# Optimization experiments

Hardware: AMD Instinct MI355X
Metric: run time of the kernel (lower is better)

Reference implementation:

```python
import jax, jax.numpy as jnp
import numpy as np

B, S, DM, DC, L, NS = 4, 2048, 2048, 512, 4, 5  # batch, seq, d_model, d_cortical, n_layers, n_settle


def _ln(x, g, b):
    # torch nn.LayerNorm, eps=1e-5
    m = x.mean(-1, keepdims=True)
    v = ((x - m) ** 2).mean(-1, keepdims=True)
    return (x - m) * jax.lax.rsqrt(v + 1e-5) * g + b


def setup_inputs() -> dict:
    key = jax.random.key(0)
    ks = jax.random.split(key, 20)
    f = lambda k, sh: jax.random.normal(k, sh, jnp.float32) * 0.02
    return dict(
        qwen_final_hidden=jax.random.normal(ks[0], (B, S, DM), jnp.float32),
        obs=jax.random.normal(ks[1], (4, B, S, DM), jnp.float32),
        proj_W=f(ks[2], (4, DC, DM)), proj_b=f(ks[3], (4, DC)),
        fuse_W=f(ks[4], (DC, 4 * DC)), fuse_b=f(ks[5], (DC,)),
        up_W=f(ks[6], (L, DC, DC)), up_b=f(ks[7], (L, DC)),
        lateral_W=f(ks[8], (L, DC, DC)), lateral_b=f(ks[9], (L, DC)),
        precision_logit=f(ks[10], (L, DC)),
        ln_g=jnp.ones((L, DC), jnp.float32), ln_b=jnp.zeros((L, DC), jnp.float32),
        down_W=f(ks[11], (L - 1, DC, DC)), down_b=f(ks[12], (L - 1, DC)),
        out1_W=f(ks[13], (DC, DC)), out1_b=f(ks[14], (DC,)),
        out2_W=f(ks[15], (DM, DC)), out2_b=f(ks[16], (DM,)),
    )


def reference(qwen_final_hidden, obs, proj_W, proj_b, fuse_W, fuse_b,
              up_W, up_b, lateral_W, lateral_b, precision_logit,
              ln_g, ln_b, down_W, down_b, out1_W, out1_b, out2_W, out2_b):
    b, s, dm = qwen_final_hidden.shape
    # per-observed-layer input projections, concatenated along features
    proj = jnp.einsum('obsd,ocd->bsoc', obs, proj_W) + proj_b  # (B,S,4,DC)
    cat = proj.reshape(b, s, -1)
    fused = cat @ fuse_W.T + fuse_b                             # (B,S,DC)
    x0 = fused.reshape(b * s, DC)                               # per-token cortical input

    prec = jax.nn.sigmoid(precision_logit)                      # (L,DC)

    # initial bottom-up pass: activations = compress(x)
    acts = []
    x = x0
    for i in range(L):
        x = _ln(x @ up_W[i].T + up_b[i], ln_g[i], ln_b[i])
        acts.append(x)

    # settling iterations
    for _ in range(NS):
        # top-down predictions computed from pre-sweep activations
        preds = [None] * L
        for i in range(L - 1, 0, -1):
            if i < L - 1:  # top layer has no top-down weights
                preds[i - 1] = acts[i] @ down_W[i].T + down_b[i]
        x = x0
        for i in range(L):
            compressed = _ln(x @ up_W[i].T + up_b[i], ln_g[i], ln_b[i])
            target = preds[i] if preds[i] is not None else acts[i]
            werr = (compressed - target) * prec[i]
            lateral = acts[i] @ lateral_W[i].T + lateral_b[i]
            acts[i] = _ln(acts[i] + 0.5 * werr + 0.1 * lateral, ln_g[i], ln_b[i])
            x = acts[i]

    top = acts[-1]
    h = jax.nn.gelu(top @ out1_W.T + out1_b, approximate=False)
    correction = (h @ out2_W.T + out2_b).reshape(b, s, dm)
    return qwen_final_hidden + correction
```

## Files before the change

### kernel.cpp

```cpp
#include <hip/hip_runtime.h>
#include <hip/hip_bf16.h>
#include <math.h>

#define NTOK 8192
#define DMD  2048
#define DCC  512
#define TOKH 4194304

typedef __attribute__((ext_vector_type(8))) short short8;
typedef __attribute__((ext_vector_type(4))) float f32x4;

__device__ inline float bf2f(unsigned short u) {
    union { unsigned int i; float f; } x; x.i = ((unsigned int)u) << 16; return x.f;
}
__device__ inline unsigned short f2bf(float f) {
    union { float f; unsigned int i; } x; x.f = f;
    unsigned int u = x.i;
    return (unsigned short)((u + 0x7fffu + ((u >> 16) & 1u)) >> 16);
}

typedef const __attribute__((address_space(1))) unsigned int* gas1_t;
typedef __attribute__((address_space(3))) unsigned int* las3_t;
__device__ inline void async16(const void* g, void* l) {
    __builtin_amdgcn_global_load_lds(
        (gas1_t)g,
        (las3_t)(unsigned int)(unsigned long long)l, 16, 0, 0);
}

__global__ __launch_bounds__(256)
void cvt_kernel(const float* __restrict__ s, unsigned short* __restrict__ d, int n4)
{
    int i = blockIdx.x * 256 + threadIdx.x;
    if (i >= n4) return;
    float4 v = ((const float4*)s)[i];
    ushort4 o;
    o.x = f2bf(v.x); o.y = f2bf(v.y); o.z = f2bf(v.z); o.w = f2bf(v.w);
    ((ushort4*)d)[i] = o;
}

struct CvtArgs { const float* src[7]; };

__global__ __launch_bounds__(256)
void wcvt_kernel(CvtArgs ca, unsigned short* __restrict__ dst)
{
    const int total = 2359296;
    for (int i = blockIdx.x * 256 + threadIdx.x; i < total; i += gridDim.x * 256) {
        const float* sp; int base;
        if      (i < 1048576) { sp = ca.src[0]; base = 0;       }
        else if (i < 1310720) { sp = ca.src[1]; base = 1048576; }
        else if (i < 1572864) { sp = ca.src[2]; base = 1310720; }
        else if (i < 1835008) { sp = ca.src[3]; base = 1572864; }
        else if (i < 2031616) { sp = ca.src[4]; base = 1835008; }
        else if (i < 2097152) { sp = ca.src[5]; base = 2031616; }
        else                  { sp = ca.src[6]; base = 2097152; }
        float4 v = ((const float4*)sp)[i - base];
        ushort4 o;
        o.x = f2bf(v.x); o.y = f2bf(v.y); o.z = f2bf(v.z); o.w = f2bf(v.w);
        ((ushort4*)dst)[i] = o;
    }
}

struct GArgs {
    const unsigned short* A[6];
    const unsigned short* W[6];
    const float*          bias[6];
    const float*          add[6];
    void*                 C[6];
};

template<bool OUTF32, bool GELU>
__global__ __launch_bounds__(256)
void gemm16(GArgs ga, int lda, int ldw, int ldadd, int ldc, int K)
{
    __shared__ unsigned short As[128 * 32];
    __shared__ unsigned short Bs[128 * 32];

    const int z    = blockIdx.z;
    const int tid  = threadIdx.x;
    const int wave = tid >> 6;
    const int lane = tid & 63;

    const int nwg   = gridDim.x * gridDim.y;
    const int bid   = blockIdx.y * gridDim.x + blockIdx.x;
    const int swz   = (bid & 7) * (nwg >> 3) + (bid >> 3);
    const int bn    = (swz % gridDim.x) * 128;
    const int bm    = (swz / gridDim.x) * 128;

    const int wr   = wave >> 1;
    const int wc   = wave & 1;

    const unsigned short* Ap = ga.A[z];
    const unsigned short* Wp = ga.W[z];

    const int lrow = lane >> 2;
    const int lcol = (lane & 3) * 8;

    f32x4 acc[4][4] = {};

    for (int k0 = 0; k0 < K; k0 += 32) {
        #pragma unroll
        for (int r = 0; r < 2; ++r) {
            int c = wave + r * 4;
            async16(Ap + (size_t)(bm + c * 16 + lrow) * lda + k0 + lcol, As + c * 512);
            async16(Wp + (size_t)(bn + c * 16 + lrow) * ldw + k0 + lcol, Bs + c * 512);
        }
        __syncthreads();

        short8 af[4], bfr[4];
        #pragma unroll
        for (int i = 0; i < 4; ++i) {
            af[i]  = *(const short8*)&As[(wr * 64 + i * 16 + (lane & 15)) * 32 + (lane >> 4) * 8];
            bfr[i] = *(const short8*)&Bs[(wc * 64 + i * 16 + (lane & 15)) * 32 + (lane >> 4) * 8];
        }
        #pragma unroll
        for (int mi = 0; mi < 4; ++mi)
            #pragma unroll
            for (int ni = 0; ni < 4; ++ni)
                acc[mi][ni] = __builtin_amdgcn_mfma_f32_16x16x32_bf16(
                    af[mi], bfr[ni], acc[mi][ni], 0, 0, 0);
        __syncthreads();
    }

    const float* bias = ga.bias[z];
    const float* add  = ga.add[z];
    #pragma unroll
    for (int ni = 0; ni < 4; ++ni) {
        int col = bn + wc * 64 + ni * 16 + (lane & 15);
        float bv = bias ? bias[col] : 0.0f;
        #pragma unroll
        for (int mi = 0; mi < 4; ++mi) {
            #pragma unroll
            for (int r = 0; r < 4; ++r) {
                int row = bm + wr * 64 + mi * 16 + (lane >> 4) * 4 + r;
                float vv = acc[mi][ni][r] + bv;
                if (GELU) vv = 0.5f * vv * (1.0f + erff(vv * 0.7071067811865475f));
                if (OUTF32) {
                    if (add) vv += add[(size_t)row * ldadd + col];
                    ((float*)ga.C[z])[(size_t)row * ldc + col] = vv;
                } else {
                    ((unsigned short*)ga.C[z])[(size_t)row * ldc + col] = f2bf(vv);
                }
            }
        }
    }
}

__device__ inline int csw(int rl, int col) {
    return rl * 512 + (col ^ (((rl >> 2) & 3) << 4));
}

template<int MODE>
__global__ __launch_bounds__(256)
void gemm_fused(const unsigned short* __restrict__ Ap,
                const unsigned short* __restrict__ Wp,
                const float* __restrict__ bias,
                const float* __restrict__ g,
                const float* __restrict__ b,
                const unsigned short* a_in,
                const unsigned short* t_in,
                const unsigned short* __restrict__ lat_in,
                const float* __restrict__ logit,
                unsigned short* outp)
{
    __shared__ unsigned short As[2][32 * 32];
    __shared__ unsigned short Bs[2][512 * 32];
    __shared__ float red[2][4][32];

    const int tid  = threadIdx.x;
    const int wave = tid >> 6;
    const int lane = tid & 63;
    const int lrow = lane >> 2;
    const int lc8  = (lane & 3) * 8;
    const int bm   = blockIdx.x * 32;
    const int l15  = lane & 15;
    const int lh   = lane >> 4;

    f32x4 acc[2][8] = {};

    if (wave < 2)
        async16(Ap + (size_t)(bm + wave * 16 + lrow) * DCC + lc8, &As[0][wave * 512]);
    #pragma unroll
    for (int r = 0; r < 8; ++r)
        async16(Wp + (size_t)((r * 4 + wave) * 16 + lrow) * DCC + lc8,
                &Bs[0][(r * 4 + wave) * 512]);
    __syncthreads();

    for (int t = 0; t < 16; ++t) {
        const int cur = t & 1;
        if (t < 15) {
            const int k0 = (t + 1) * 32;
            if (wave < 2)
                async16(Ap + (size_t)(bm + wave * 16 + lrow) * DCC + k0 + lc8,
                        &As[cur ^ 1][wave * 512]);
            #pragma unroll
            for (int r = 0; r < 8; ++r)
                async16(Wp + (size_t)((r * 4 + wave) * 16 + lrow) * DCC + k0 + lc8,
                        &Bs[cur ^ 1][(r * 4 + wave) * 512]);
        }
        short8 af[2], bfr[8];
        #pragma unroll
        for (int mi = 0; mi < 2; ++mi)
            af[mi] = *(const short8*)&As[cur][(mi * 16 + l15) * 32 + lh * 8];
        #pragma unroll
        for (int ni = 0; ni < 8; ++ni)
            bfr[ni] = *(const short8*)&Bs[cur][(wave * 128 + ni * 16 + l15) * 32 + lh * 8];
        #pragma unroll
        for (int mi = 0; mi < 2; ++mi)
            #pragma unroll
            for (int ni = 0; ni < 8; ++ni)
                acc[mi][ni] = __builtin_amdgcn_mfma_f32_16x16x32_bf16(
                    af[mi], bfr[ni], acc[mi][ni], 0, 0, 0);
        __syncthreads();
    }

    float bv[8], gv[8], bbv[8];
    #pragma unroll
    for (int ni = 0; ni < 8; ++ni) {
        int col = wave * 128 + ni * 16 + l15;
        bv[ni] = bias[col]; gv[ni] = g[col]; bbv[ni] = b[col];
    }

    float ps[2][4], pq[2][4];
    #pragma unroll
    for (int mi = 0; mi < 2; ++mi)
        #pragma unroll
        for (int rr = 0; rr < 4; ++rr) {
            float s = 0.f, q = 0.f;
            #pragma unroll
            for (int ni = 0; ni < 8; ++ni) {
                float v = acc[mi][ni][rr] + bv[ni];
                acc[mi][ni][rr] = v;
                s += v; q += v * v;
            }
            #pragma unroll
            for (int off = 1; off < 16; off <<= 1) {
                s += __shfl_xor(s, off, 64);
                q += __shfl_xor(q, off, 64);
            }
            ps[mi][rr] = s; pq[mi][rr] = q;
        }
    if (l15 == 0) {
        #pragma unroll
        for (int mi = 0; mi < 2; ++mi)
            #pragma unroll
            for (int rr = 0; rr < 4; ++rr) {
                int rl = mi * 16 + lh * 4 + rr;
                red[0][wave][rl] = ps[mi][rr];
                red[1][wave][rl] = pq[mi][rr];
            }
    }
    __syncthreads();

    unsigned short* compS = &Bs[0][0];
    #pragma unroll
    for (int mi = 0; mi < 2; ++mi)
        #pragma unroll
        for (int rr = 0; rr < 4; ++rr) {
            int rl = mi * 16 + lh * 4 + rr;
            float s = red[0][0][rl] + red[0][1][rl] + red[0][2][rl] + red[0][3][rl];
            float q = red[1][0][rl] + red[1][1][rl] + red[1][2][rl] + red[1][3][rl];
            float m1 = s * (1.0f / DCC);
            float r1 = rsqrtf(q * (1.0f / DCC) - m1 * m1 + 1e-5f);
            #pragma unroll
            for (int ni = 0; ni < 8; ++ni) {
                int col = wave * 128 + ni * 16 + l15;
                compS[csw(rl, col)] = f2bf((acc[mi][ni][rr] - m1) * r1 * gv[ni] + bbv[ni]);
            }
        }
    __syncthreads();

    float gr[8], br[8], pr[8];
    if constexpr (MODE == 1) {
        const int c0 = lane * 8;
        float4 g0 = *(const float4*)(g + c0),     g1 = *(const float4*)(g + c0 + 4);
        float4 b0 = *(const float4*)(b + c0),     b1 = *(const float4*)(b + c0 + 4);
        float4 p0 = *(const float4*)(logit + c0), p1 = *(const float4*)(logit + c0 + 4);
        float gt[8] = {g0.x,g0.y,g0.z,g0.w,g1.x,g1.y,g1.z,g1.w};
        float bt[8] = {b0.x,b0.y,b0.z,b0.w,b1.x,b1.y,b1.z,b1.w};
        float pt[8] = {p0.x,p0.y,p0.z,p0.w,p1.x,p1.y,p1.z,p1.w};
        #pragma unroll
        for (int j = 0; j < 8; ++j) {
            gr[j] = gt[j]; br[j] = bt[j];
            pr[j] = 1.0f / (1.0f + __expf(-pt[j]));
        }
    }

    #pragma unroll
    for (int rr = 0; rr < 8; ++rr) {
        const int rl = wave * 8 + rr;
        const size_t gbase = (size_t)(bm + rl) * DCC + lane * 8;
        short8 cm = *(const short8*)&compS[csw(rl, lane * 8)];
        if constexpr (MODE == 0) {
            *(short8*)(outp + gbase) = cm;
        } else {
            short8 ar = *(const short8*)(a_in + gbase);
            short8 tr = *(const short8*)(t_in + gbase);
            short8 lr = *(const short8*)(lat_in + gbase);
            float tv[8], s = 0.f, q = 0.f;
            #pragma unroll
            for (int j = 0; j < 8; ++j) {
                float val = bf2f((unsigned short)ar[j])
                          + 0.5f * (bf2f((unsigned short)cm[j]) - bf2f((unsigned short)tr[j])) * pr[j]
                          + 0.1f * bf2f((unsigned short)lr[j]);
                tv[j] = val; s += val; q += val * val;
            }
            #pragma unroll
            for (int off = 1; off < 64; off <<= 1) {
                s += __shfl_xor(s, off, 64);
                q += __shfl_xor(q, off, 64);
            }
            float m2 = s * (1.0f / DCC);
            float r2 = rsqrtf(q * (1.0f / DCC) - m2 * m2 + 1e-5f);
            short8 o;
            #pragma unroll
            for (int j = 0; j < 8; ++j)
                o[j] = (short)f2bf((tv[j] - m2) * r2 * gr[j] + br[j]);
            *(short8*)(outp + gbase) = o;
        }
    }
}

extern "C" void kernel_launch(void* const* d_in, const int* in_sizes, int n_in,
                              void* d_out, int out_size, void* d_ws, size_t ws_size,
                              hipStream_t stream)
{
    const float* qwen   = (const float*)d_in[0];
    const float* obs    = (const float*)d_in[1];
    const float* proj_W = (const float*)d_in[2];
    const float* proj_b = (const float*)d_in[3];
    const float* fuse_W = (const float*)d_in[4];
    const float* fuse_b = (const float*)d_in[5];
    const float* up_W   = (const float*)d_in[6];
    const float* up_b   = (const float*)d_in[7];
    const float* lat_W  = (const float*)d_in[8];
    const float* lat_b  = (const float*)d_in[9];
    const float* plogit = (const float*)d_in[10];
    const float* ln_g   = (const float*)d_in[11];
    const float* ln_b   = (const float*)d_in[12];
    const float* down_W = (const float*)d_in[13];
    const float* down_b = (const float*)d_in[14];
    const float* out1_W = (const float*)d_in[15];
    const float* out1_b = (const float*)d_in[16];
    const float* out2_W = (const float*)d_in[17];
    const float* out2_b = (const float*)d_in[18];
    float* out = (float*)d_out;

    unsigned short* wsu = (unsigned short*)d_ws;
    unsigned short* catbuf = wsu;
    unsigned short* x0b    = wsu + 16777216;
    unsigned short* acts16[4] = {
        wsu + 20971520, wsu + 20971520 + TOKH,
        wsu + 20971520 + 2 * TOKH, wsu + 20971520 + 3 * TOKH };
    unsigned short* w16    = wsu + 37748736;
    unsigned short* projW16 = w16;
    unsigned short* fuseW16 = w16 + 4194304;
    unsigned short* upW16   = w16 + 5242880;
    unsigned short* latW16  = w16 + 6291456;
    unsigned short* downW16 = w16 + 7340032;
    unsigned short* out1W16 = w16 + 8126464;
    unsigned short* out2W16 = w16 + 8388608;
    unsigned short* h16     = catbuf;

    unsigned short* outu = (unsigned short*)d_out;
    unsigned short* pred16a = outu;
    unsigned short* pred16b = outu + TOKH;
    unsigned short* lat16[4] = { outu + 2*TOKH, outu + 3*TOKH, outu + 4*TOKH, outu + 5*TOKH };

    dim3 blk(256);

    {
        CvtArgs ca;
        ca.src[0] = proj_W; ca.src[1] = fuse_W; ca.src[2] = up_W;
        ca.src[3] = lat_W;  ca.src[4] = down_W; ca.src[5] = out1_W;
        ca.src[6] = out2_W;
        wcvt_kernel<<<dim3(2048), blk, 0, stream>>>(ca, w16);
    }

    for (int p = 0; p < 2; ++p) {
        int n4 = (2 * NTOK * DMD) / 4;
        cvt_kernel<<<dim3((n4 + 255) / 256), blk, 0, stream>>>(
            obs + (size_t)p * 2 * NTOK * DMD, outu, n4);
        GArgs a{};
        for (int q = 0; q < 2; ++q) {
            int o = 2 * p + q;
            a.A[q]    = outu + (size_t)q * NTOK * DMD;
            a.W[q]    = projW16 + (size_t)o * DCC * DMD;
            a.bias[q] = proj_b + o * DCC;
            a.C[q]    = catbuf + o * DCC;
        }
        gemm16<false, false><<<dim3(DCC/128, NTOK/128, 2), blk, 0, stream>>>(
            a, DMD, DMD, 0, 4 * DCC, DMD);
    }
    {
        GArgs a{};
        a.A[0] = catbuf; a.W[0] = fuseW16; a.bias[0] = fuse_b; a.C[0] = x0b;
        gemm16<false, false><<<dim3(DCC/128, NTOK/128, 1), blk, 0, stream>>>(
            a, 4 * DCC, 4 * DCC, 0, DCC, 4 * DCC);
    }

    for (int i = 0; i < 4; ++i) {
        gemm_fused<0><<<dim3(NTOK/32), blk, 0, stream>>>(
            (i == 0) ? x0b : acts16[i - 1],
            upW16 + (size_t)i * DCC * DCC, up_b + i * DCC,
            ln_g + i * DCC, ln_b + i * DCC,
            nullptr, nullptr, nullptr, nullptr, acts16[i]);
    }

    for (int s = 0; s < 5; ++s) {
        {
            GArgs a{};
            a.A[0] = acts16[1]; a.W[0] = downW16 + (size_t)1 * DCC * DCC;
            a.bias[0] = down_b + 1 * DCC; a.C[0] = pred16a;
            a.A[1] = acts16[2]; a.W[1] = downW16 + (size_t)2 * DCC * DCC;
            a.bias[1] = down_b + 2 * DCC; a.C[1] = pred16b;
            for (int i = 0; i < 4; ++i) {
                a.A[2 + i] = acts16[i];
                a.W[2 + i] = latW16 + (size_t)i * DCC * DCC;
                a.bias[2 + i] = lat_b + i * DCC;
                a.C[2 + i] = lat16[i];
            }
            gemm16<false, false><<<dim3(DCC/128, NTOK/128, 6), blk, 0, stream>>>(
                a, DCC, DCC, 0, DCC, DCC);
        }
        for (int i = 0; i < 4; ++i) {
            const unsigned short* tgt =
                (i == 0) ? pred16a : (i == 1) ? pred16b : acts16[i];
            gemm_fused<1><<<dim3(NTOK/32), blk, 0, stream>>>(
                (i == 0) ? x0b : acts16[i - 1],
                upW16 + (size_t)i * DCC * DCC, up_b + i * DCC,
                ln_g + i * DCC, ln_b + i * DCC,
                acts16[i], tgt, lat16[i], plogit + i * DCC, acts16[i]);
        }
    }

    {
        GArgs a{};
        a.A[0] = acts16[3]; a.W[0] = out1W16; a.bias[0] = out1_b; a.C[0] = h16;
        gemm16<false, true><<<dim3(DCC/128, NTOK/128, 1), blk, 0, stream>>>(
            a, DCC, DCC, 0, DCC, DCC);
    }
    {
        GArgs a{};
        a.A[0] = h16; a.W[0] = out2W16; a.bias[0] = out2_b;
        a.add[0] = qwen; a.C[0] = out;
        gemm16<true, false><<<dim3(DMD/128, NTOK/128, 1), blk, 0, stream>>>(
            a, DCC, DCC, DMD, DMD, DCC);
    }
}
```

Measured before the change: 1.595 ms.

## Fuse lateral, down-projection and out1 GEMMs into the per-layer settle kernel

Each settle-layer kernel now computes its lateral GEMM in-block into shared memory, then optionally runs an appended GEMM on the fresh activation tile: down-projection for the next iteration's prediction, or out1 with GELU on the last step. This removes the separate batched lateral/down GEMM launch and the global round-trips of the lateral and prediction buffers. It also skips the unused target load for upper layers, converts all of obs in one pass into a dedicated workspace, runs the projection GEMMs as a single launch, and changes the LDS swizzle. In exchange the fused kernel uses much more shared memory (likely fewer resident blocks) and does serial GEMMs per block.

```diff
diff --git a/kernel.cpp b/kernel.cpp
--- a/kernel.cpp
+++ b/kernel.cpp
@@ -6,6 +6,7 @@
 #define DMD  2048
 #define DCC  512
 #define TOKH 4194304
+#define WSZ  262144
 
 typedef __attribute__((ext_vector_type(8))) short short8;
 typedef __attribute__((ext_vector_type(4))) float f32x4;
@@ -146,24 +147,31 @@
 }
 
 __device__ inline int csw(int rl, int col) {
-    return rl * 512 + (col ^ (((rl >> 2) & 3) << 4));
-}
-
-template<int MODE>
+    int s = ((rl >> 2) & 3) ^ (rl & 3);
+    return rl * 512 + (col ^ (s << 4));
+}
+
+template<bool SETTLE, bool TGTG, int APPEND>
 __global__ __launch_bounds__(256)
 void gemm_fused(const unsigned short* __restrict__ Ap,
-                const unsigned short* __restrict__ Wp,
-                const float* __restrict__ bias,
+                const unsigned short* __restrict__ upW,
+                const float* __restrict__ up_bias,
                 const float* __restrict__ g,
                 const float* __restrict__ b,
                 const unsigned short* a_in,
                 const unsigned short* t_in,
-                const unsigned short* __restrict__ lat_in,
+                const unsigned short* __restrict__ latW,
+                const float* __restrict__ lat_bias,
                 const float* __restrict__ logit,
-                unsigned short* outp)
+                unsigned short* outp,
+                const unsigned short* __restrict__ apW,
+                const float* __restrict__ ap_bias,
+                unsigned short* ap_out)
 {
-    __shared__ unsigned short As[2][32 * 32];
     __shared__ unsigned short Bs[2][512 * 32];
+    __shared__ unsigned short As2[2][32 * 32];
+    __shared__ unsigned short compS[32 * 512];
+    __shared__ unsigned short latS[32 * 512];
     __shared__ float red[2][4][32];
 
     const int tid  = threadIdx.x;
@@ -175,49 +183,70 @@
     const int l15  = lane & 15;
     const int lh   = lane >> 4;
 
-    f32x4 acc[2][8] = {};
-
-    if (wave < 2)
-        async16(Ap + (size_t)(bm + wave * 16 + lrow) * DCC + lc8, &As[0][wave * 512]);
-    #pragma unroll
-    for (int r = 0; r < 8; ++r)
-        async16(Wp + (size_t)((r * 4 + wave) * 16 + lrow) * DCC + lc8,
-                &Bs[0][(r * 4 + wave) * 512]);
-    __syncthreads();
-
-    for (int t = 0; t < 16; ++t) {
-        const int cur = t & 1;
-        if (t < 15) {
-            const int k0 = (t + 1) * 32;
-            if (wave < 2)
-                async16(Ap + (size_t)(bm + wave * 16 + lrow) * DCC + k0 + lc8,
-                        &As[cur ^ 1][wave * 512]);
-            #pragma unroll
-            for (int r = 0; r < 8; ++r)
-                async16(Wp + (size_t)((r * 4 + wave) * 16 + lrow) * DCC + k0 + lc8,
-                        &Bs[cur ^ 1][(r * 4 + wave) * 512]);
-        }
-        short8 af[2], bfr[8];
+    f32x4 acc[2][8];
+
+    auto run = [&](const unsigned short* Ag, const unsigned short* Wg) {
         #pragma unroll
         for (int mi = 0; mi < 2; ++mi)
-            af[mi] = *(const short8*)&As[cur][(mi * 16 + l15) * 32 + lh * 8];
-        #pragma unroll
-        for (int ni = 0; ni < 8; ++ni)
-            bfr[ni] = *(const short8*)&Bs[cur][(wave * 128 + ni * 16 + l15) * 32 + lh * 8];
-        #pragma unroll
-        for (int mi = 0; mi < 2; ++mi)
             #pragma unroll
             for (int ni = 0; ni < 8; ++ni)
-                acc[mi][ni] = __builtin_amdgcn_mfma_f32_16x16x32_bf16(
-                    af[mi], bfr[ni], acc[mi][ni], 0, 0, 0);
+                acc[mi][ni] = f32x4{0.f, 0.f, 0.f, 0.f};
+        if (wave < 2)
+            async16(Ag + (size_t)(bm + wave * 16 + lrow) * DCC + lc8, &As2[0][wave * 512]);
+        #pragma unroll
+        for (int r = 0; r < 8; ++r)
+            async16(Wg + (size_t)((r * 4 + wave) * 16 + lrow) * DCC + lc8,
+                    &Bs[0][(r * 4 + wave) * 512]);
         __syncthreads();
-    }
+        for (int t = 0; t < 16; ++t) {
+            const int cur = t & 1;
+            if (t < 15) {
+                const int k0 = (t + 1) * 32;
+                if (wave < 2)
+                    async16(Ag + (size_t)(bm + wave * 16 + lrow) * DCC + k0 + lc8,
+                            &As2[cur ^ 1][wave * 512]);
+                #pragma unroll
+                for (int r = 0; r < 8; ++r)
+                    async16(Wg + (size_t)((r * 4 + wave) * 16 + lrow) * DCC + k0 + lc8,
+                            &Bs[cur ^ 1][(r * 4 + wave) * 512]);
+            }
+            short8 af[2];
+            #pragma unroll
+            for (int mi = 0; mi < 2; ++mi)
+                af[mi] = *(const short8*)&As2[cur][(mi * 16 + l15) * 32 + lh * 8];
+            #pragma unroll
+            for (int ni = 0; ni < 8; ++ni) {
+                short8 bf8 = *(const short8*)&Bs[cur][(wave * 128 + ni * 16 + l15) * 32 + lh * 8];
+                #pragma unroll
+                for (int mi = 0; mi < 2; ++mi)
+                    acc[mi][ni] = __builtin_amdgcn_mfma_f32_16x16x32_bf16(
+                        af[mi], bf8, acc[mi][ni], 0, 0, 0);
+            }
+            __syncthreads();
+        }
+    };
+
+    if constexpr (SETTLE) {
+        run(a_in, latW);
+        #pragma unroll
+        for (int ni = 0; ni < 8; ++ni) {
+            int col = wave * 128 + ni * 16 + l15;
+            float lb = lat_bias[col];
+            #pragma unroll
+            for (int mi = 0; mi < 2; ++mi)
+                #pragma unroll
+                for (int rr = 0; rr < 4; ++rr)
+                    latS[csw(mi * 16 + lh * 4 + rr, col)] = f2bf(acc[mi][ni][rr] + lb);
+        }
+    }
+
+    run(Ap, upW);
 
     float bv[8], gv[8], bbv[8];
     #pragma unroll
     for (int ni = 0; ni < 8; ++ni) {
         int col = wave * 128 + ni * 16 + l15;
-        bv[ni] = bias[col]; gv[ni] = g[col]; bbv[ni] = b[col];
+        bv[ni] = up_bias[col]; gv[ni] = g[col]; bbv[ni] = b[col];
     }
 
     float ps[2][4], pq[2][4];
@@ -251,7 +280,6 @@
     }
     __syncthreads();
 
-    unsigned short* compS = &Bs[0][0];
     #pragma unroll
     for (int mi = 0; mi < 2; ++mi)
         #pragma unroll
@@ -269,39 +297,46 @@
         }
     __syncthreads();
 
-    float gr[8], br[8], pr[8];
-    if constexpr (MODE == 1) {
-        const int c0 = lane * 8;
-        float4 g0 = *(const float4*)(g + c0),     g1 = *(const float4*)(g + c0 + 4);
-        float4 b0 = *(const float4*)(b + c0),     b1 = *(const float4*)(b + c0 + 4);
-        float4 p0 = *(const float4*)(logit + c0), p1 = *(const float4*)(logit + c0 + 4);
-        float gt[8] = {g0.x,g0.y,g0.z,g0.w,g1.x,g1.y,g1.z,g1.w};
-        float bt[8] = {b0.x,b0.y,b0.z,b0.w,b1.x,b1.y,b1.z,b1.w};
-        float pt[8] = {p0.x,p0.y,p0.z,p0.w,p1.x,p1.y,p1.z,p1.w};
-        #pragma unroll
-        for (int j = 0; j < 8; ++j) {
-            gr[j] = gt[j]; br[j] = bt[j];
-            pr[j] = 1.0f / (1.0f + __expf(-pt[j]));
-        }
-    }
-
-    #pragma unroll
-    for (int rr = 0; rr < 8; ++rr) {
-        const int rl = wave * 8 + rr;
-        const size_t gbase = (size_t)(bm + rl) * DCC + lane * 8;
-        short8 cm = *(const short8*)&compS[csw(rl, lane * 8)];
-        if constexpr (MODE == 0) {
+    const int c0 = lane * 8;
+    if constexpr (!SETTLE) {
+        #pragma unroll
+        for (int rr = 0; rr < 8; ++rr) {
+            const int rl = wave * 8 + rr;
+            const size_t gbase = (size_t)(bm + rl) * DCC + c0;
+            short8 cm = *(const short8*)&compS[csw(rl, c0)];
             *(short8*)(outp + gbase) = cm;
-        } else {
+        }
+    } else {
+        float gr[8], br[8], pr[8];
+        {
+            float4 g0 = *(const float4*)(g + c0),     g1 = *(const float4*)(g + c0 + 4);
+            float4 b0 = *(const float4*)(b + c0),     b1 = *(const float4*)(b + c0 + 4);
+            float4 p0 = *(const float4*)(logit + c0), p1 = *(const float4*)(logit + c0 + 4);
+            float gt[8] = {g0.x,g0.y,g0.z,g0.w,g1.x,g1.y,g1.z,g1.w};
+            float bt[8] = {b0.x,b0.y,b0.z,b0.w,b1.x,b1.y,b1.z,b1.w};
+            float pt[8] = {p0.x,p0.y,p0.z,p0.w,p1.x,p1.y,p1.z,p1.w};
+            #pragma unroll
+            for (int j = 0; j < 8; ++j) {
+                gr[j] = gt[j]; br[j] = bt[j];
+                pr[j] = 1.0f / (1.0f + __expf(-pt[j]));
+            }
+        }
+        #pragma unroll
+        for (int rr = 0; rr < 8; ++rr) {
+            const int rl = wave * 8 + rr;
+            const size_t gbase = (size_t)(bm + rl) * DCC + c0;
+            short8 cm = *(const short8*)&compS[csw(rl, c0)];
+            short8 lm = *(const short8*)&latS[csw(rl, c0)];
             short8 ar = *(const short8*)(a_in + gbase);
-            short8 tr = *(const short8*)(t_in + gbase);
-            short8 lr = *(const short8*)(lat_in + gbase);
+            short8 tr;
+            if constexpr (TGTG) tr = *(const short8*)(t_in + gbase);
+            else                tr = ar;
             float tv[8], s = 0.f, q = 0.f;
             #pragma unroll
             for (int j = 0; j < 8; ++j) {
                 float val = bf2f((unsigned short)ar[j])
                           + 0.5f * (bf2f((unsigned short)cm[j]) - bf2f((unsigned short)tr[j])) * pr[j]
-                          + 0.1f * bf2f((unsigned short)lr[j]);
+                          + 0.1f * bf2f((unsigned short)lm[j]);
                 tv[j] = val; s += val; q += val * val;
             }
             #pragma unroll
@@ -316,6 +351,60 @@
             for (int j = 0; j < 8; ++j)
                 o[j] = (short)f2bf((tv[j] - m2) * r2 * gr[j] + br[j]);
             *(short8*)(outp + gbase) = o;
+            if constexpr (APPEND > 0)
+                *(short8*)&compS[csw(rl, c0)] = o;
+        }
+    }
+
+    if constexpr (APPEND > 0) {
+        __syncthreads();
+        #pragma unroll
+        for (int mi = 0; mi < 2; ++mi)
+            #pragma unroll
+            for (int ni = 0; ni < 8; ++ni)
+                acc[mi][ni] = f32x4{0.f, 0.f, 0.f, 0.f};
+        #pragma unroll
+        for (int r = 0; r < 8; ++r)
+            async16(apW + (size_t)((r * 4 + wave) * 16 + lrow) * DCC + lc8,
+                    &Bs[0][(r * 4 + wave) * 512]);
+        __syncthreads();
+        for (int t = 0; t < 16; ++t) {
+            const int cur = t & 1;
+            if (t < 15) {
+                const int k0 = (t + 1) * 32;
+                #pragma unroll
+                for (int r = 0; r < 8; ++r)
+                    async16(apW + (size_t)((r * 4 + wave) * 16 + lrow) * DCC + k0 + lc8,
+                            &Bs[cur ^ 1][(r * 4 + wave) * 512]);
+            }
+            short8 af[2];
+            #pragma unroll
+            for (int mi = 0; mi < 2; ++mi)
+                af[mi] = *(const short8*)&compS[csw(mi * 16 + l15, t * 32 + lh * 8)];
+            #pragma unroll
+            for (int ni = 0; ni < 8; ++ni) {
+                short8 bf8 = *(const short8*)&Bs[cur][(wave * 128 + ni * 16 + l15) * 32 + lh * 8];
+                #pragma unroll
+                for (int mi = 0; mi < 2; ++mi)
+                    acc[mi][ni] = __builtin_amdgcn_mfma_f32_16x16x32_bf16(
+                        af[mi], bf8, acc[mi][ni], 0, 0, 0);
+            }
+            __syncthreads();
+        }
+        #pragma unroll
+        for (int ni = 0; ni < 8; ++ni) {
+            int col = wave * 128 + ni * 16 + l15;
+            float ab = ap_bias[col];
+            #pragma unroll
+            for (int mi = 0; mi < 2; ++mi)
+                #pragma unroll
+                for (int rr = 0; rr < 4; ++rr) {
+                    int row = bm + mi * 16 + lh * 4 + rr;
+                    float vv = acc[mi][ni][rr] + ab;
+                    if (APPEND == 2)
+                        vv = 0.5f * vv * (1.0f + erff(vv * 0.7071067811865475f));
+                    ap_out[(size_t)row * DCC + col] = f2bf(vv);
+                }
         }
     }
 }
@@ -359,12 +448,12 @@
     unsigned short* downW16 = w16 + 7340032;
     unsigned short* out1W16 = w16 + 8126464;
     unsigned short* out2W16 = w16 + 8388608;
+    unsigned short* obs16   = wsu + 47185920;
     unsigned short* h16     = catbuf;
 
     unsigned short* outu = (unsigned short*)d_out;
     unsigned short* pred16a = outu;
     unsigned short* pred16b = outu + TOKH;
-    unsigned short* lat16[4] = { outu + 2*TOKH, outu + 3*TOKH, outu + 4*TOKH, outu + 5*TOKH };
 
     dim3 blk(256);
 
@@ -376,19 +465,17 @@
         wcvt_kernel<<<dim3(2048), blk, 0, stream>>>(ca, w16);
     }
 
-    for (int p = 0; p < 2; ++p) {
-        int n4 = (2 * NTOK * DMD) / 4;
-        cvt_kernel<<<dim3((n4 + 255) / 256), blk, 0, stream>>>(
-            obs + (size_t)p * 2 * NTOK * DMD, outu, n4);
+    {
+        int n4 = (4 * NTOK * DMD) / 4;
+        cvt_kernel<<<dim3(n4 / 256), blk, 0, stream>>>(obs, obs16, n4);
         GArgs a{};
-        for (int q = 0; q < 2; ++q) {
-            int o = 2 * p + q;
-            a.A[q]    = outu + (size_t)q * NTOK * DMD;
-            a.W[q]    = projW16 + (size_t)o * DCC * DMD;
-            a.bias[q] = proj_b + o * DCC;
-            a.C[q]    = catbuf + o * DCC;
-        }
-        gemm16<false, false><<<dim3(DCC/128, NTOK/128, 2), blk, 0, stream>>>(
+        for (int o = 0; o < 4; ++o) {
+            a.A[o]    = obs16 + (size_t)o * NTOK * DMD;
+            a.W[o]    = projW16 + (size_t)o * DCC * DMD;
+            a.bias[o] = proj_b + o * DCC;
+            a.C[o]    = catbuf + o * DCC;
+        }
+        gemm16<false, false><<<dim3(DCC/128, NTOK/128, 4), blk, 0, stream>>>(
             a, DMD, DMD, 0, 4 * DCC, DMD);
     }
     {
@@ -398,47 +485,62 @@
             a, 4 * DCC, 4 * DCC, 0, DCC, 4 * DCC);
     }
 
-    for (int i = 0; i < 4; ++i) {
-        gemm_fused<0><<<dim3(NTOK/32), blk, 0, stream>>>(
-            (i == 0) ? x0b : acts16[i - 1],
-            upW16 + (size_t)i * DCC * DCC, up_b + i * DCC,
-            ln_g + i * DCC, ln_b + i * DCC,
-            nullptr, nullptr, nullptr, nullptr, acts16[i]);
-    }
+    dim3 fgrid(NTOK / 32);
+
+    gemm_fused<false, false, 0><<<fgrid, blk, 0, stream>>>(
+        x0b, upW16, up_b, ln_g, ln_b,
+        nullptr, nullptr, nullptr, nullptr, nullptr, acts16[0],
+        nullptr, nullptr, nullptr);
+    gemm_fused<false, false, 1><<<fgrid, blk, 0, stream>>>(
+        acts16[0], upW16 + WSZ, up_b + DCC, ln_g + DCC, ln_b + DCC,
+        nullptr, nullptr, nullptr, nullptr, nullptr, acts16[1],
+        downW16 + WSZ, down_b + DCC, pred16a);
+    gemm_fused<false, false, 1><<<fgrid, blk, 0, stream>>>(
+        acts16[1], upW16 + 2 * WSZ, up_b + 2 * DCC, ln_g + 2 * DCC, ln_b + 2 * DCC,
+        nullptr, nullptr, nullptr, nullptr, nullptr, acts16[2],
+        downW16 + 2 * WSZ, down_b + 2 * DCC, pred16b);
+    gemm_fused<false, false, 0><<<fgrid, blk, 0, stream>>>(
+        acts16[2], upW16 + 3 * WSZ, up_b + 3 * DCC, ln_g + 3 * DCC, ln_b + 3 * DCC,
+        nullptr, nullptr, nullptr, nullptr, nullptr, acts16[3],
+        nullptr, nullptr, nullptr);
 
     for (int s = 0; s < 5; ++s) {
-        {
-            GArgs a{};
-            a.A[0] = acts16[1]; a.W[0] = downW16 + (size_t)1 * DCC * DCC;
-            a.bias[0] = down_b + 1 * DCC; a.C[0] = pred16a;
-            a.A[1] = acts16[2]; a.W[1] = downW16 + (size_t)2 * DCC * DCC;
-            a.bias[1] = down_b + 2 * DCC; a.C[1] = pred16b;
-            for (int i = 0; i < 4; ++i) {
-                a.A[2 + i] = acts16[i];
-                a.W[2 + i] = latW16 + (size_t)i * DCC * DCC;
-                a.bias[2 + i] = lat_b + i * DCC;
-                a.C[2 + i] = lat16[i];
-            }
-            gemm16<false, false><<<dim3(DCC/128, NTOK/128, 6), blk, 0, stream>>>(
-                a, DCC, DCC, 0, DCC, DCC);
-        }
-        for (int i = 0; i < 4; ++i) {
-            const unsigned short* tgt =
-                (i == 0) ? pred16a : (i == 1) ? pred16b : acts16[i];
-            gemm_fused<1><<<dim3(NTOK/32), blk, 0, stream>>>(
-                (i == 0) ? x0b : acts16[i - 1],
-                upW16 + (size_t)i * DCC * DCC, up_b + i * DCC,
-                ln_g + i * DCC, ln_b + i * DCC,
-                acts16[i], tgt, lat16[i], plogit + i * DCC, acts16[i]);
-        }
-    }
-
-    {
-        GArgs a{};
-        a.A[0] = acts16[3]; a.W[0] = out1W16; a.bias[0] = out1_b; a.C[0] = h16;
-        gemm16<false, true><<<dim3(DCC/128, NTOK/128, 1), blk, 0, stream>>>(
-            a, DCC, DCC, 0, DCC, DCC);
-    }
+        gemm_fused<true, true, 0><<<fgrid, blk, 0, stream>>>(
+            x0b, upW16, up_b, ln_g, ln_b,
+            acts16[0], pred16a, latW16, lat_b, plogit, acts16[0],
+            nullptr, nullptr, nullptr);
+        if (s < 4)
+            gemm_fused<true, true, 1><<<fgrid, blk, 0, stream>>>(
+                acts16[0], upW16 + WSZ, up_b + DCC, ln_g + DCC, ln_b + DCC,
+                acts16[1], pred16b, latW16 + WSZ, lat_b + DCC, plogit + DCC, acts16[1],
+                downW16 + WSZ, down_b + DCC, pred16a);
+        else
+            gemm_fused<true, true, 0><<<fgrid, blk, 0, stream>>>(
+                acts16[0], upW16 + WSZ, up_b + DCC, ln_g + DCC, ln_b + DCC,
+                acts16[1], pred16b, latW16 + WSZ, lat_b + DCC, plogit + DCC, acts16[1],
+                nullptr, nullptr, nullptr);
+        if (s < 4)
+            gemm_fused<true, false, 1><<<fgrid, blk, 0, stream>>>(
+                acts16[1], upW16 + 2 * WSZ, up_b + 2 * DCC, ln_g + 2 * DCC, ln_b + 2 * DCC,
+                acts16[2], nullptr, latW16 + 2 * WSZ, lat_b + 2 * DCC, plogit + 2 * DCC, acts16[2],
+                downW16 + 2 * WSZ, down_b + 2 * DCC, pred16b);
+        else
+            gemm_fused<true, false, 0><<<fgrid, blk, 0, stream>>>(
+                acts16[1], upW16 + 2 * WSZ, up_b + 2 * DCC, ln_g + 2 * DCC, ln_b + 2 * DCC,
+                acts16[2], nullptr, latW16 + 2 * WSZ, lat_b + 2 * DCC, plogit + 2 * DCC, acts16[2],
+                nullptr, nullptr, nullptr);
+        if (s < 4)
+            gemm_fused<true, false, 0><<<fgrid, blk, 0, stream>>>(
+                acts16[2], upW16 + 3 * WSZ, up_b + 3 * DCC, ln_g + 3 * DCC, ln_b + 3 * DCC,
+                acts16[3], nullptr, latW16 + 3 * WSZ, lat_b + 3 * DCC, plogit + 3 * DCC, acts16[3],
+                nullptr, nullptr, nullptr);
+        else
+            gemm_fused<true, false, 2><<<fgrid, blk, 0, stream>>>(
+                acts16[2], upW16 + 3 * WSZ, up_b + 3 * DCC, ln_g + 3 * DCC, ln_b + 3 * DCC,
+                acts16[3], nullptr, latW16 + 3 * WSZ, lat_b + 3 * DCC, plogit + 3 * DCC, acts16[3],
+                out1W16, out1_b, h16);
+    }
+
     {
         GArgs a{};
         a.A[0] = h16; a.W[0] = out2W16; a.bias[0] = out2_b;
```

Result: slower. 1.807 ms (+13.3%).

## Use 512-thread blocks in fused LN GEMM and batch all obs projections

Applied to the files above, without the earlier changes.

The fused up-projection+LayerNorm kernel now runs 8 waves per block, each owning 64 output columns instead of 128. This halves per-wave accumulators and B-fragment loads, and the cross-wave reduction is widened to 8 waves. The compS swizzle also XORs in the low row bits to cut LDS bank conflicts. Separately, all four obs tensors are converted in one launch into a dedicated workspace and projected in a single batched GEMM launch instead of two rounds. This trades more workspace memory for fewer launches and better parallelism.

```diff
diff --git a/kernel.cpp b/kernel.cpp
--- a/kernel.cpp
+++ b/kernel.cpp
@@ -146,11 +146,12 @@
 }
 
 __device__ inline int csw(int rl, int col) {
-    return rl * 512 + (col ^ (((rl >> 2) & 3) << 4));
+    int s = ((rl >> 2) & 3) ^ (rl & 3);
+    return rl * 512 + (col ^ (s << 4));
 }
 
 template<int MODE>
-__global__ __launch_bounds__(256)
+__global__ __launch_bounds__(512)
 void gemm_fused(const unsigned short* __restrict__ Ap,
                 const unsigned short* __restrict__ Wp,
                 const float* __restrict__ bias,
@@ -162,9 +163,9 @@
                 const float* __restrict__ logit,
                 unsigned short* outp)
 {
-    __shared__ unsigned short As[2][32 * 32];
     __shared__ unsigned short Bs[2][512 * 32];
-    __shared__ float red[2][4][32];
+    __shared__ unsigned short As2[2][32 * 32];
+    __shared__ float red[2][8][32];
 
     const int tid  = threadIdx.x;
     const int wave = tid >> 6;
@@ -175,14 +176,14 @@
     const int l15  = lane & 15;
     const int lh   = lane >> 4;
 
-    f32x4 acc[2][8] = {};
+    f32x4 acc[2][4] = {};
 
     if (wave < 2)
-        async16(Ap + (size_t)(bm + wave * 16 + lrow) * DCC + lc8, &As[0][wave * 512]);
+        async16(Ap + (size_t)(bm + wave * 16 + lrow) * DCC + lc8, &As2[0][wave * 512]);
     #pragma unroll
-    for (int r = 0; r < 8; ++r)
-        async16(Wp + (size_t)((r * 4 + wave) * 16 + lrow) * DCC + lc8,
-                &Bs[0][(r * 4 + wave) * 512]);
+    for (int r = 0; r < 4; ++r)
+        async16(Wp + (size_t)((r * 8 + wave) * 16 + lrow) * DCC + lc8,
+                &Bs[0][(r * 8 + wave) * 512]);
     __syncthreads();
 
     for (int t = 0; t < 16; ++t) {
@@ -191,32 +192,32 @@
             const int k0 = (t + 1) * 32;
             if (wave < 2)
                 async16(Ap + (size_t)(bm + wave * 16 + lrow) * DCC + k0 + lc8,
-                        &As[cur ^ 1][wave * 512]);
-            #pragma unroll
-            for (int r = 0; r < 8; ++r)
-                async16(Wp + (size_t)((r * 4 + wave) * 16 + lrow) * DCC + k0 + lc8,
-                        &Bs[cur ^ 1][(r * 4 + wave) * 512]);
-        }
-        short8 af[2], bfr[8];
+                        &As2[cur ^ 1][wave * 512]);
+            #pragma unroll
+            for (int r = 0; r < 4; ++r)
+                async16(Wp + (size_t)((r * 8 + wave) * 16 + lrow) * DCC + k0 + lc8,
+                        &Bs[cur ^ 1][(r * 8 + wave) * 512]);
+        }
+        short8 af[2], bfr[4];
         #pragma unroll
         for (int mi = 0; mi < 2; ++mi)
-            af[mi] = *(const short8*)&As[cur][(mi * 16 + l15) * 32 + lh * 8];
-        #pragma unroll
-        for (int ni = 0; ni < 8; ++ni)
-            bfr[ni] = *(const short8*)&Bs[cur][(wave * 128 + ni * 16 + l15) * 32 + lh * 8];
+            af[mi] = *(const short8*)&As2[cur][(mi * 16 + l15) * 32 + lh * 8];
+        #pragma unroll
+        for (int ni = 0; ni < 4; ++ni)
+            bfr[ni] = *(const short8*)&Bs[cur][(wave * 64 + ni * 16 + l15) * 32 + lh * 8];
         #pragma unroll
         for (int mi = 0; mi < 2; ++mi)
             #pragma unroll
-            for (int ni = 0; ni < 8; ++ni)
+            for (int ni = 0; ni < 4; ++ni)
                 acc[mi][ni] = __builtin_amdgcn_mfma_f32_16x16x32_bf16(
                     af[mi], bfr[ni], acc[mi][ni], 0, 0, 0);
         __syncthreads();
     }
 
-    float bv[8], gv[8], bbv[8];
+    float bv[4], gv[4], bbv[4];
     #pragma unroll
-    for (int ni = 0; ni < 8; ++ni) {
-        int col = wave * 128 + ni * 16 + l15;
+    for (int ni = 0; ni < 4; ++ni) {
+        int col = wave * 64 + ni * 16 + l15;
         bv[ni] = bias[col]; gv[ni] = g[col]; bbv[ni] = b[col];
     }
 
@@ -227,7 +228,7 @@
         for (int rr = 0; rr < 4; ++rr) {
             float s = 0.f, q = 0.f;
             #pragma unroll
-            for (int ni = 0; ni < 8; ++ni) {
+            for (int ni = 0; ni < 4; ++ni) {
                 float v = acc[mi][ni][rr] + bv[ni];
                 acc[mi][ni][rr] = v;
                 s += v; q += v * v;
@@ -257,42 +258,48 @@
         #pragma unroll
         for (int rr = 0; rr < 4; ++rr) {
             int rl = mi * 16 + lh * 4 + rr;
-            float s = red[0][0][rl] + red[0][1][rl] + red[0][2][rl] + red[0][3][rl];
-            float q = red[1][0][rl] + red[1][1][rl] + red[1][2][rl] + red[1][3][rl];
+            float s = 0.f, q = 0.f;
+            #pragma unroll
+            for (int w = 0; w < 8; ++w) { s += red[0][w][rl]; q += red[1][w][rl]; }
             float m1 = s * (1.0f / DCC);
             float r1 = rsqrtf(q * (1.0f / DCC) - m1 * m1 + 1e-5f);
             #pragma unroll
-            for (int ni = 0; ni < 8; ++ni) {
-                int col = wave * 128 + ni * 16 + l15;
+            for (int ni = 0; ni < 4; ++ni) {
+                int col = wave * 64 + ni * 16 + l15;
                 compS[csw(rl, col)] = f2bf((acc[mi][ni][rr] - m1) * r1 * gv[ni] + bbv[ni]);
             }
         }
     __syncthreads();
 
-    float gr[8], br[8], pr[8];
-    if constexpr (MODE == 1) {
-        const int c0 = lane * 8;
-        float4 g0 = *(const float4*)(g + c0),     g1 = *(const float4*)(g + c0 + 4);
-        float4 b0 = *(const float4*)(b + c0),     b1 = *(const float4*)(b + c0 + 4);
-        float4 p0 = *(const float4*)(logit + c0), p1 = *(const float4*)(logit + c0 + 4);
-        float gt[8] = {g0.x,g0.y,g0.z,g0.w,g1.x,g1.y,g1.z,g1.w};
-        float bt[8] = {b0.x,b0.y,b0.z,b0.w,b1.x,b1.y,b1.z,b1.w};
-        float pt[8] = {p0.x,p0.y,p0.z,p0.w,p1.x,p1.y,p1.z,p1.w};
-        #pragma unroll
-        for (int j = 0; j < 8; ++j) {
-            gr[j] = gt[j]; br[j] = bt[j];
-            pr[j] = 1.0f / (1.0f + __expf(-pt[j]));
-        }
-    }
-
-    #pragma unroll
-    for (int rr = 0; rr < 8; ++rr) {
-        const int rl = wave * 8 + rr;
-        const size_t gbase = (size_t)(bm + rl) * DCC + lane * 8;
-        short8 cm = *(const short8*)&compS[csw(rl, lane * 8)];
-        if constexpr (MODE == 0) {
+    const int c0 = lane * 8;
+    if constexpr (MODE == 0) {
+        #pragma unroll
+        for (int rr = 0; rr < 4; ++rr) {
+            const int rl = wave * 4 + rr;
+            const size_t gbase = (size_t)(bm + rl) * DCC + c0;
+            short8 cm = *(const short8*)&compS[csw(rl, c0)];
             *(short8*)(outp + gbase) = cm;
-        } else {
+        }
+    } else {
+        float gr[8], br[8], pr[8];
+        {
+            float4 g0 = *(const float4*)(g + c0),     g1 = *(const float4*)(g + c0 + 4);
+            float4 b0 = *(const float4*)(b + c0),     b1 = *(const float4*)(b + c0 + 4);
+            float4 p0 = *(const float4*)(logit + c0), p1 = *(const float4*)(logit + c0 + 4);
+            float gt[8] = {g0.x,g0.y,g0.z,g0.w,g1.x,g1.y,g1.z,g1.w};
+            float bt[8] = {b0.x,b0.y,b0.z,b0.w,b1.x,b1.y,b1.z,b1.w};
+            float pt[8] = {p0.x,p0.y,p0.z,p0.w,p1.x,p1.y,p1.z,p1.w};
+            #pragma unroll
+            for (int j = 0; j < 8; ++j) {
+                gr[j] = gt[j]; br[j] = bt[j];
+                pr[j] = 1.0f / (1.0f + __expf(-pt[j]));
+            }
+        }
+        #pragma unroll
+        for (int rr = 0; rr < 4; ++rr) {
+            const int rl = wave * 4 + rr;
+            const size_t gbase = (size_t)(bm + rl) * DCC + c0;
+            short8 cm = *(const short8*)&compS[csw(rl, c0)];
             short8 ar = *(const short8*)(a_in + gbase);
             short8 tr = *(const short8*)(t_in + gbase);
             short8 lr = *(const short8*)(lat_in + gbase);
@@ -359,6 +366,7 @@
     unsigned short* downW16 = w16 + 7340032;
     unsigned short* out1W16 = w16 + 8126464;
     unsigned short* out2W16 = w16 + 8388608;
+    unsigned short* obs16   = wsu + 47185920;
     unsigned short* h16     = catbuf;
 
     unsigned short* outu = (unsigned short*)d_out;
@@ -367,6 +375,7 @@
     unsigned short* lat16[4] = { outu + 2*TOKH, outu + 3*TOKH, outu + 4*TOKH, outu + 5*TOKH };
 
     dim3 blk(256);
+    dim3 blk512(512);
 
     {
         CvtArgs ca;
@@ -376,19 +385,17 @@
         wcvt_kernel<<<dim3(2048), blk, 0, stream>>>(ca, w16);
     }
 
-    for (int p = 0; p < 2; ++p) {
-        int n4 = (2 * NTOK * DMD) / 4;
-        cvt_kernel<<<dim3((n4 + 255) / 256), blk, 0, stream>>>(
-            obs + (size_t)p * 2 * NTOK * DMD, outu, n4);
+    {
+        int n4 = (4 * NTOK * DMD) / 4;
+        cvt_kernel<<<dim3(n4 / 256), blk, 0, stream>>>(obs, obs16, n4);
         GArgs a{};
-        for (int q = 0; q < 2; ++q) {
-            int o = 2 * p + q;
-            a.A[q]    = outu + (size_t)q * NTOK * DMD;
-            a.W[q]    = projW16 + (size_t)o * DCC * DMD;
-            a.bias[q] = proj_b + o * DCC;
-            a.C[q]    = catbuf + o * DCC;
-        }
-        gemm16<false, false><<<dim3(DCC/128, NTOK/128, 2), blk, 0, stream>>>(
+        for (int o = 0; o < 4; ++o) {
+            a.A[o]    = obs16 + (size_t)o * NTOK * DMD;
+            a.W[o]    = projW16 + (size_t)o * DCC * DMD;
+            a.bias[o] = proj_b + o * DCC;
+            a.C[o]    = catbuf + o * DCC;
+        }
+        gemm16<false, false><<<dim3(DCC/128, NTOK/128, 4), blk, 0, stream>>>(
             a, DMD, DMD, 0, 4 * DCC, DMD);
     }
     {
@@ -398,8 +405,10 @@
             a, 4 * DCC, 4 * DCC, 0, DCC, 4 * DCC);
     }
 
+    dim3 fgrid(NTOK / 32);
+
     for (int i = 0; i < 4; ++i) {
-        gemm_fused<0><<<dim3(NTOK/32), blk, 0, stream>>>(
+        gemm_fused<0><<<fgrid, blk512, 0, stream>>>(
             (i == 0) ? x0b : acts16[i - 1],
             upW16 + (size_t)i * DCC * DCC, up_b + i * DCC,
             ln_g + i * DCC, ln_b + i * DCC,
@@ -425,7 +434,7 @@
         for (int i = 0; i < 4; ++i) {
             const unsigned short* tgt =
                 (i == 0) ? pred16a : (i == 1) ? pred16b : acts16[i];
-            gemm_fused<1><<<dim3(NTOK/32), blk, 0, stream>>>(
+            gemm_fused<1><<<fgrid, blk512, 0, stream>>>(
                 (i == 0) ? x0b : acts16[i - 1],
                 upW16 + (size_t)i * DCC * DCC, up_b + i * DCC,
                 ln_g + i * DCC, ln_b + i * DCC,
```

Measured after the change: 1.574 ms. About the same (-1.3%).
